# Optimization experiments

Hardware: AMD Instinct MI355X
Metric: run time of the kernel (lower is better)

Reference implementation:

```python
import jax, jax.numpy as jnp
from jax import lax
import numpy as np

DN = ('NCHW', 'OIHW', 'NCHW')


def _conv(x, w, b):
    y = lax.conv_general_dilated(x, w, (1, 1), 'SAME', dimension_numbers=DN)
    return y + b[None, :, None, None]


def setup_inputs() -> dict:
    key = jax.random.key(0)
    ks = jax.random.split(key, 8)
    B = 2
    noise = 0.1 * jax.random.normal(ks[0], (B, 768, 577), dtype=jnp.float32)  # N(0, 0.1)
    targets = jax.random.randint(ks[1], (B, 384, 384), 0, 171)
    w1 = 0.02 * jax.random.normal(ks[2], (512, 768, 3, 3), dtype=jnp.float32)
    b1 = 0.02 * jax.random.normal(ks[3], (512,), dtype=jnp.float32)
    w2 = 0.02 * jax.random.normal(ks[4], (512, 512, 3, 3), dtype=jnp.float32)
    b2 = 0.02 * jax.random.normal(ks[5], (512,), dtype=jnp.float32)
    w3 = 0.2 * jax.random.normal(ks[6], (77,), dtype=jnp.float32)  # Con3: Conv2d(1,77,1x1)
    b3 = 0.2 * jax.random.normal(ks[7], (77,), dtype=jnp.float32)
    return {'noise': noise, 'targets': targets, 'w1': w1, 'b1': b1,
            'w2': w2, 'b2': b2, 'w3': w3, 'b3': b3}


def reference(noise, targets, w1, b1, w2, b2, w3, b3):
    B = noise.shape[0]
    # NoiseToImage is shadowed by an empty nn.Sequential() -> identity
    image_noise = jnp.transpose(noise, (2, 0, 1))  # (577, B, 768)

    # --- NoiseToText ---
    H, W = targets.shape[1], targets.shape[2]
    ih = (jnp.arange(24) * H) // 24  # nearest-neighbor interpolate indices
    iw = (jnp.arange(24) * W) // 24
    m = targets[:, ih][:, :, iw]  # (B, 24, 24) class labels
    # one-hot scatter into 256 channels, keep first 171 (labels >=171 -> all-zero)
    mask = (m[:, None] == jnp.arange(171)[None, :, None, None]).astype(noise.dtype)  # (B,171,24,24)

    x = noise[:, :, 1:].reshape(B, 768, 24, 24)  # drop CLS token
    xm = x[:, None] * mask[:, :, None]            # (B,171,768,24,24)
    xm = xm.reshape(B * 171, 768, 24, 24)

    y = _conv(xm, w1, b1)                         # (B*171,512,24,24)
    y = y.reshape(-1, 512, 6, 4, 6, 4).mean(axis=(3, 5))  # AdaptiveAvgPool2d((6,6))
    y = _conv(y, w2, b2)                          # (B*171,512,6,6)
    y = y.mean(axis=(2, 3))                       # AdaptiveAvgPool2d((1,1)) -> (B*171,512)
    y = y.reshape(B, 171, 1, 512).transpose(0, 2, 1, 3)  # (B,1,171,512)
    # Con3: 1x1 conv with in_channels=1, out_channels=77
    text_noise = w3[None, :, None, None] * y + b3[None, :, None, None]  # (B,77,171,512)
    return image_noise, text_noise
```

## Files before the change

### kernel.cpp

```cpp
#include <hip/hip_runtime.h>
#include <hip/hip_bf16.h>

typedef unsigned short u16;
typedef short bf16x8 __attribute__((ext_vector_type(8)));
typedef float f32x4 __attribute__((ext_vector_type(4)));

__device__ __forceinline__ u16 f2bf(float f){
    unsigned u = __float_as_uint(f);
    unsigned r = 0x7fffu + ((u >> 16) & 1u);
    return (u16)((u + r) >> 16);
}

__device__ __forceinline__ void gload_lds16(const u16* g, u16* lds_base){
    __builtin_amdgcn_global_load_lds(
        (const __attribute__((address_space(1))) unsigned int*)g,
        (__attribute__((address_space(3))) unsigned int*)lds_base, 16, 0, 0);
}

#define OUT0_N 886272
#define OUT1_N 13483008
#define YN 175104
#define KS2 24

__global__ void k_prep(const float* __restrict__ noise, const int* __restrict__ targets,
                       const float* __restrict__ w1, const float* __restrict__ b1,
                       const float* __restrict__ w2, const float* __restrict__ b2,
                       float* __restrict__ out0, u16* __restrict__ XbfT,
                       u16* __restrict__ Are, u16* __restrict__ Mfull16,
                       float* __restrict__ bias, int* __restrict__ labels,
                       u16* __restrict__ Zcat16){
    __shared__ float sh[32 * 33];
    int blk = blockIdx.x;
    int tid = threadIdx.x;
    if (blk < 912){
        int b   = blk / 456;
        int rem = blk % 456;
        int cb  = rem / 19, sb = rem % 19;
        int tx = tid & 31, ty = tid >> 5;
        int s0 = sb * 32, c0 = cb * 32;
        float (*tile)[33] = (float(*)[33])sh;
        #pragma unroll
        for (int i = 0; i < 4; i++){
            int c = c0 + ty + i * 8;
            int s = s0 + tx;
            if (s < 577) tile[ty + i * 8][tx] = noise[(size_t)(b * 768 + c) * 577 + s];
        }
        __syncthreads();
        #pragma unroll
        for (int i = 0; i < 4; i++){
            int s = s0 + ty + i * 8;
            int c = c0 + tx;
            if (s >= 577) continue;
            float v = tile[tx][ty + i * 8];
            out0[(size_t)(s * 2 + b) * 768 + c] = v;
            if (s >= 1) XbfT[(size_t)(b * 576 + s - 1) * 768 + c] = f2bf(v);
        }
    } else if (blk < 2448){
        int idx = (blk - 912) * 256 + tid;
        int k = idx % 768; int c1 = idx / 768;
        const float* wp = w1 + (size_t)idx * 9;
        #pragma unroll
        for (int tap = 0; tap < 9; tap++)
            Are[(size_t)(c1 * 9 + tap) * 768 + k] = f2bf(wp[tap]);
    } else if (blk < 3472){
        int idx = (blk - 2448) * 256 + tid;
        int c1 = idx % 512, c2 = idx / 512;
        const float* wp = w2 + (size_t)(c2 * 512 + c1) * 9;
        float t[3][3];
        #pragma unroll
        for (int r = 0; r < 3; r++)
            #pragma unroll
            for (int s = 0; s < 3; s++)
                t[r][s] = wp[r * 3 + s];
        float cs0[3], cs1[3], cs2[3];
        #pragma unroll
        for (int r = 0; r < 3; r++){
            cs0[r] = t[r][0] + t[r][1];
            cs1[r] = t[r][0] + t[r][1] + t[r][2];
            cs2[r] = t[r][1] + t[r][2];
        }
        const float inv = 1.0f / 576.0f;
        u16* Mp = Mfull16 + (size_t)(c2 * 512 + c1) * 9;
        Mp[0] = f2bf(inv * (cs0[0] + cs0[1]));
        Mp[1] = f2bf(inv * (cs1[0] + cs1[1]));
        Mp[2] = f2bf(inv * (cs2[0] + cs2[1]));
        Mp[3] = f2bf(inv * (cs0[0] + cs0[1] + cs0[2]));
        Mp[4] = f2bf(inv * (cs1[0] + cs1[1] + cs1[2]));
        Mp[5] = f2bf(inv * (cs2[0] + cs2[1] + cs2[2]));
        Mp[6] = f2bf(inv * (cs0[1] + cs0[2]));
        Mp[7] = f2bf(inv * (cs1[1] + cs1[2]));
        Mp[8] = f2bf(inv * (cs2[1] + cs2[2]));
    } else if (blk < 3984){
        int c2 = blk - 3472;
        const float cw[9] = {25.f,30.f,25.f,30.f,36.f,30.f,25.f,30.f,25.f};
        float sb = 0.f;
        for (int c1 = tid; c1 < 512; c1 += 256){
            const float* wp = w2 + (size_t)(c2 * 512 + c1) * 9;
            float s = 0.f;
            #pragma unroll
            for (int q = 0; q < 9; q++) s += wp[q] * cw[q];
            sb += b1[c1] * s;
        }
        sh[tid] = sb; __syncthreads();
        for (int o = 128; o > 0; o >>= 1){ if (tid < o) sh[tid] += sh[tid + o]; __syncthreads(); }
        if (tid == 0) bias[c2] = b2[c2] + sh[0] * (1.0f / 36.0f);
    } else if (blk < 3989){
        int idx = (blk - 3984) * 256 + tid;
        if (idx < 1152){
            int b = idx / 576; int p = idx % 576;
            int i = p / 24, j = p % 24;
            labels[idx] = targets[b * 147456 + i * 16 * 384 + j * 16];
        }
    } else {
        int idx = (blk - 3989) * 256 + tid;
        if (idx < 193536) Zcat16[342 * 4608 + idx] = 0;
    }
}

__launch_bounds__(256)
__global__ void k_gemm1(const u16* __restrict__ Are, const u16* __restrict__ XbfT,
                        float* __restrict__ D){
    __shared__ u16 As[128 * 64];
    __shared__ u16 Bs[64 * 64];
    int tid  = threadIdx.x;
    int wave = tid >> 6, lane = tid & 63;
    int l16 = lane & 15, quad = lane >> 4;
    int wm = wave >> 1, wn = wave & 1;
    int m0 = blockIdx.x * 128;
    int n0 = blockIdx.y * 64;
    int srow = lane >> 3, scol = (lane & 7) * 8;
    f32x4 acc[4][2] = {};
    for (int k0 = 0; k0 < 768; k0 += 64){
        #pragma unroll
        for (int j = 0; j < 4; j++){
            int ch = wave * 4 + j;
            gload_lds16(Are + (size_t)(m0 + ch * 8 + srow) * 768 + k0 + scol, &As[ch * 512]);
        }
        #pragma unroll
        for (int j = 0; j < 2; j++){
            int ch = wave * 2 + j;
            gload_lds16(XbfT + (size_t)(n0 + ch * 8 + srow) * 768 + k0 + scol, &Bs[ch * 512]);
        }
        __syncthreads();
        #pragma unroll
        for (int ks = 0; ks < 2; ks++){
            bf16x8 af[4], bf[2];
            #pragma unroll
            for (int i = 0; i < 4; i++)
                af[i] = *(const bf16x8*)&As[(wm * 64 + i * 16 + l16) * 64 + ks * 32 + quad * 8];
            #pragma unroll
            for (int i = 0; i < 2; i++)
                bf[i] = *(const bf16x8*)&Bs[(wn * 32 + i * 16 + l16) * 64 + ks * 32 + quad * 8];
            #pragma unroll
            for (int mi = 0; mi < 4; mi++)
                #pragma unroll
                for (int ni = 0; ni < 2; ni++)
                    acc[mi][ni] = __builtin_amdgcn_mfma_f32_16x16x32_bf16(af[mi], bf[ni], acc[mi][ni], 0, 0, 0);
        }
        __syncthreads();
    }
    #pragma unroll
    for (int mi = 0; mi < 4; mi++)
        #pragma unroll
        for (int ni = 0; ni < 2; ni++)
            #pragma unroll
            for (int r = 0; r < 4; r++)
                D[(size_t)(m0 + wm * 64 + mi * 16 + quad * 4 + r) * 1152 + n0 + wn * 32 + ni * 16 + l16] = acc[mi][ni][r];
}

__launch_bounds__(256)
__global__ void k_scatter(const float* __restrict__ D, const int* __restrict__ labels,
                          u16* __restrict__ Zcat16){
    int blk = blockIdx.x;
    int b  = blk >> 9;
    int c1 = blk & 511;
    __shared__ float acc[171 * 9];
    int t = threadIdx.x;
    for (int q = t; q < 1539; q += 256) acc[q] = 0.f;
    __syncthreads();
    for (int p = t; p < 576; p += 256){
        int cls = labels[b * 576 + p];
        if (cls < 0 || cls >= 171) continue;
        int i = p / 24, j = p % 24;
        float slot[9];
        #pragma unroll
        for (int q = 0; q < 9; q++) slot[q] = 0.f;
        unsigned used = 0;
        int tau[3]; bool vs[3];
        #pragma unroll
        for (int s1 = 0; s1 < 3; s1++){
            int v = j - s1 + 1;
            vs[s1]  = (v >= 0 && v < 24);
            tau[s1] = (v < 4) ? 0 : ((v < 20) ? 1 : 2);
        }
        #pragma unroll
        for (int r1 = 0; r1 < 3; r1++){
            int u = i - r1 + 1;
            if (u < 0 || u >= 24) continue;
            int rho = (u < 4) ? 0 : ((u < 20) ? 1 : 2);
            #pragma unroll
            for (int s1 = 0; s1 < 3; s1++){
                if (!vs[s1]) continue;
                float tv = D[(size_t)(c1 * 9 + r1 * 3 + s1) * 1152 + b * 576 + p];
                int sl = rho * 3 + tau[s1];
                slot[sl] += tv;
                used |= 1u << sl;
            }
        }
        #pragma unroll
        for (int sl = 0; sl < 9; sl++)
            if (used & (1u << sl)) atomicAdd(&acc[cls * 9 + sl], slot[sl]);
    }
    __syncthreads();
    for (int q = t; q < 1539; q += 256){
        int cls = q / 9, sl = q % 9;
        Zcat16[(size_t)(b * 171 + cls) * 4608 + c1 * 9 + sl] = f2bf(acc[q]);
    }
}

__launch_bounds__(256)
__global__ void k_gemm2m(const u16* __restrict__ Zcat16, const u16* __restrict__ Mfull16,
                         float* __restrict__ ypart){
    __shared__ u16 As[128 * 64];
    __shared__ u16 Bs[64 * 64];
    int tid  = threadIdx.x;
    int wave = tid >> 6, lane = tid & 63;
    int l16 = lane & 15, quad = lane >> 4;
    int wm = wave >> 1, wn = wave & 1;
    int m0 = blockIdx.x * 128;
    int n0 = blockIdx.y * 64;
    int kbeg = blockIdx.z * 192;
    int srow = lane >> 3, scol = (lane & 7) * 8;
    f32x4 acc[4][2] = {};
    for (int k0 = kbeg; k0 < kbeg + 192; k0 += 64){
        #pragma unroll
        for (int j = 0; j < 4; j++){
            int ch = wave * 4 + j;
            gload_lds16(Zcat16 + (size_t)(m0 + ch * 8 + srow) * 4608 + k0 + scol, &As[ch * 512]);
        }
        #pragma unroll
        for (int j = 0; j < 2; j++){
            int ch = wave * 2 + j;
            gload_lds16(Mfull16 + (size_t)(n0 + ch * 8 + srow) * 4608 + k0 + scol, &Bs[ch * 512]);
        }
        __syncthreads();
        #pragma unroll
        for (int ks = 0; ks < 2; ks++){
            bf16x8 af[4], bf[2];
            #pragma unroll
            for (int i = 0; i < 4; i++)
                af[i] = *(const bf16x8*)&As[(wm * 64 + i * 16 + l16) * 64 + ks * 32 + quad * 8];
            #pragma unroll
            for (int i = 0; i < 2; i++)
                bf[i] = *(const bf16x8*)&Bs[(wn * 32 + i * 16 + l16) * 64 + ks * 32 + quad * 8];
            #pragma unroll
            for (int mi = 0; mi < 4; mi++)
                #pragma unroll
                for (int ni = 0; ni < 2; ni++)
                    acc[mi][ni] = __builtin_amdgcn_mfma_f32_16x16x32_bf16(af[mi], bf[ni], acc[mi][ni], 0, 0, 0);
        }
        __syncthreads();
    }
    float* yp = ypart + (size_t)blockIdx.z * YN;
    #pragma unroll
    for (int mi = 0; mi < 4; mi++)
        #pragma unroll
        for (int r = 0; r < 4; r++){
            int n = m0 + wm * 64 + mi * 16 + quad * 4 + r;
            if (n >= 342) continue;
            #pragma unroll
            for (int ni = 0; ni < 2; ni++)
                yp[(size_t)n * 512 + n0 + wn * 32 + ni * 16 + l16] = acc[mi][ni][r];
        }
}

__global__ void k_finalr(const float* __restrict__ ypart, const float* __restrict__ bias,
                         const float* __restrict__ w3, const float* __restrict__ b3,
                         float4* __restrict__ out1){
    __shared__ float w3s[77], b3s[77];
    int tid = threadIdx.x;
    if (tid < 77){ w3s[tid] = w3[tid]; b3s[tid] = b3[tid]; }
    __syncthreads();
    int idx = blockIdx.x * 256 + tid;
    if (idx >= YN / 4) return;
    int c4 = idx & 127;
    int n  = idx >> 7;
    const float4* bp = (const float4*)bias;
    float4 sum = bp[c4];
    #pragma unroll 4
    for (int s = 0; s < KS2; s++){
        float4 v = *(const float4*)&ypart[(size_t)s * YN + (size_t)n * 512 + c4 * 4];
        sum.x += v.x; sum.y += v.y; sum.z += v.z; sum.w += v.w;
    }
    int b = n / 171, cls = n % 171;
    size_t base = ((size_t)b * 77 * 171 + cls) * 128 + c4;
    #pragma unroll
    for (int o = 0; o < 77; o++){
        float w = w3s[o], bb = b3s[o];
        out1[base + (size_t)o * 171 * 128] =
            make_float4(w * sum.x + bb, w * sum.y + bb, w * sum.z + bb, w * sum.w + bb);
    }
}

extern "C" void kernel_launch(void* const* d_in, const int* in_sizes, int n_in,
                              void* d_out, int out_size, void* d_ws, size_t ws_size,
                              hipStream_t stream) {
    const float* noise   = (const float*)d_in[0];
    const int*   targets = (const int*)  d_in[1];
    const float* w1      = (const float*)d_in[2];
    const float* b1      = (const float*)d_in[3];
    const float* w2      = (const float*)d_in[4];
    const float* b2      = (const float*)d_in[5];
    const float* w3      = (const float*)d_in[6];
    const float* b3      = (const float*)d_in[7];
    float* out0 = (float*)d_out;
    float* out1 = out0 + OUT0_N;

    char* ws = (char*)d_ws;
    const size_t OFF_ARE  = 0;
    const size_t OFF_X    = 7077888;
    const size_t OFF_D    = OFF_X   + 1769472;
    const size_t OFF_MF   = OFF_D   + 21233664;
    const size_t OFF_ZC   = OFF_MF  + 4718592;
    const size_t OFF_BIAS = OFF_ZC  + 3538944;
    const size_t OFF_LAB  = OFF_BIAS + 2048;

    u16*   Are    = (u16*)  (ws + OFF_ARE);
    u16*   XbfT   = (u16*)  (ws + OFF_X);
    float* D      = (float*)(ws + OFF_D);
    float* ypart  = (float*)(ws + OFF_D);
    u16*   Mfull16= (u16*)  (ws + OFF_MF);
    u16*   Zcat16 = (u16*)  (ws + OFF_ZC);
    float* bias   = (float*)(ws + OFF_BIAS);
    int*   labels = (int*)  (ws + OFF_LAB);

    k_prep  <<<4745, 256, 0, stream>>>(noise, targets, w1, b1, w2, b2,
                                       out0, XbfT, Are, Mfull16, bias, labels, Zcat16);
    k_gemm1 <<<dim3(36, 18), 256, 0, stream>>>(Are, XbfT, D);
    k_scatter<<<1024, 256, 0, stream>>>(D, labels, Zcat16);
    k_gemm2m<<<dim3(3, 8, KS2), 256, 0, stream>>>(Zcat16, Mfull16, ypart);
    k_finalr<<<171, 256, 0, stream>>>(ypart, bias, w3, b3, (float4*)out1);
}
```

Measured before the change: 157.7 us.

## Halve GEMM2 split-K and split final reduction from coalesced output expansion

The split-K factor of the second GEMM drops from 24 to 12, so each block covers twice the K range and there are fewer partial sums to write and reduce. The old final kernel, which ran on 171 blocks and issued 77 strided stores per thread, is replaced by two kernels. A small reduction kernel writes the summed y to workspace, and an expand kernel with about 13k blocks writes the 54 MB output with fully contiguous float4 stores. This targets poor parallelism and store coalescing in the output-bound last stage, at the cost of one extra launch and a smaller grid for GEMM2.

```diff
diff --git a/kernel.cpp b/kernel.cpp
--- a/kernel.cpp
+++ b/kernel.cpp
@@ -20,7 +20,7 @@
 #define OUT0_N 886272
 #define OUT1_N 13483008
 #define YN 175104
-#define KS2 24
+#define KS2 12
 
 __global__ void k_prep(const float* __restrict__ noise, const int* __restrict__ targets,
                        const float* __restrict__ w1, const float* __restrict__ b1,
@@ -229,10 +229,10 @@
     int wm = wave >> 1, wn = wave & 1;
     int m0 = blockIdx.x * 128;
     int n0 = blockIdx.y * 64;
-    int kbeg = blockIdx.z * 192;
+    int kbeg = blockIdx.z * 384;
     int srow = lane >> 3, scol = (lane & 7) * 8;
     f32x4 acc[4][2] = {};
-    for (int k0 = kbeg; k0 < kbeg + 192; k0 += 64){
+    for (int k0 = kbeg; k0 < kbeg + 384; k0 += 64){
         #pragma unroll
         for (int j = 0; j < 4; j++){
             int ch = wave * 4 + j;
@@ -274,32 +274,34 @@
         }
 }
 
-__global__ void k_finalr(const float* __restrict__ ypart, const float* __restrict__ bias,
-                         const float* __restrict__ w3, const float* __restrict__ b3,
-                         float4* __restrict__ out1){
-    __shared__ float w3s[77], b3s[77];
-    int tid = threadIdx.x;
-    if (tid < 77){ w3s[tid] = w3[tid]; b3s[tid] = b3[tid]; }
-    __syncthreads();
-    int idx = blockIdx.x * 256 + tid;
-    if (idx >= YN / 4) return;
+__global__ void k_red(const float* __restrict__ ypart, const float* __restrict__ bias,
+                      float4* __restrict__ ysum){
+    int idx = blockIdx.x * 128 + threadIdx.x;
     int c4 = idx & 127;
     int n  = idx >> 7;
-    const float4* bp = (const float4*)bias;
-    float4 sum = bp[c4];
-    #pragma unroll 4
+    float4 sum = ((const float4*)bias)[c4];
+    #pragma unroll
     for (int s = 0; s < KS2; s++){
         float4 v = *(const float4*)&ypart[(size_t)s * YN + (size_t)n * 512 + c4 * 4];
         sum.x += v.x; sum.y += v.y; sum.z += v.z; sum.w += v.w;
     }
-    int b = n / 171, cls = n % 171;
-    size_t base = ((size_t)b * 77 * 171 + cls) * 128 + c4;
-    #pragma unroll
-    for (int o = 0; o < 77; o++){
-        float w = w3s[o], bb = b3s[o];
-        out1[base + (size_t)o * 171 * 128] =
-            make_float4(w * sum.x + bb, w * sum.y + bb, w * sum.z + bb, w * sum.w + bb);
-    }
+    ysum[idx] = sum;
+}
+
+__global__ void k_expand(const float4* __restrict__ ysum, const float* __restrict__ w3,
+                         const float* __restrict__ b3, float4* __restrict__ out1){
+    int idx = blockIdx.x * 256 + threadIdx.x;
+    if (idx >= OUT1_N / 4) return;
+    int c4 = idx & 127;
+    int t  = idx >> 7;
+    int cls = t % 171;
+    int u   = t / 171;
+    int o   = u % 77;
+    int b   = u / 77;
+    float w  = w3[o];
+    float bb = b3[o];
+    float4 v = ysum[(b * 171 + cls) * 128 + c4];
+    out1[idx] = make_float4(w * v.x + bb, w * v.y + bb, w * v.z + bb, w * v.w + bb);
 }
 
 extern "C" void kernel_launch(void* const* d_in, const int* in_sizes, int n_in,
@@ -324,6 +326,7 @@
     const size_t OFF_ZC   = OFF_MF  + 4718592;
     const size_t OFF_BIAS = OFF_ZC  + 3538944;
     const size_t OFF_LAB  = OFF_BIAS + 2048;
+    const size_t OFF_YS   = OFF_LAB + 4608;
 
     u16*   Are    = (u16*)  (ws + OFF_ARE);
     u16*   XbfT   = (u16*)  (ws + OFF_X);
@@ -333,11 +336,13 @@
     u16*   Zcat16 = (u16*)  (ws + OFF_ZC);
     float* bias   = (float*)(ws + OFF_BIAS);
     int*   labels = (int*)  (ws + OFF_LAB);
+    float* ysum   = (float*)(ws + OFF_YS);
 
     k_prep  <<<4745, 256, 0, stream>>>(noise, targets, w1, b1, w2, b2,
                                        out0, XbfT, Are, Mfull16, bias, labels, Zcat16);
     k_gemm1 <<<dim3(36, 18), 256, 0, stream>>>(Are, XbfT, D);
     k_scatter<<<1024, 256, 0, stream>>>(D, labels, Zcat16);
     k_gemm2m<<<dim3(3, 8, KS2), 256, 0, stream>>>(Zcat16, Mfull16, ypart);
-    k_finalr<<<171, 256, 0, stream>>>(ypart, bias, w3, b3, (float4*)out1);
-}
+    k_red   <<<342, 128, 0, stream>>>(ypart, bias, (float4*)ysum);
+    k_expand<<<13167, 256, 0, stream>>>((const float4*)ysum, w3, b3, (float4*)out1);
+}
```

New measurement: 158.4 us. About the same (+0.4%).
